# Performance work log

Hardware: AMD Instinct MI355X
Metric: run time of the kernel (lower is better)

Reference implementation:

```python
import jax, jax.numpy as jnp
import numpy as np

SIM_THRESHOLD = 0.7
EPS = 1e-8  # matches torch F.cosine_similarity eps

Q, M, D, C = 4096, 65536, 384, 128


def setup_inputs() -> dict:
    key = jax.random.key(0)
    k1, k2, k3 = jax.random.split(key, 3)
    query_embeddings = jax.random.normal(k1, (Q, D), dtype=jnp.float32)
    memory_embeddings = jax.random.normal(k2, (M, D), dtype=jnp.float32)
    # per-example one-hot-ish label vectors [M, C]
    memory_labels = jax.random.uniform(k3, (M, C), dtype=jnp.float32)
    return {
        "query_embeddings": query_embeddings,
        "memory_embeddings": memory_embeddings,
        "memory_labels": memory_labels,
    }


def _l2_normalize(x):
    n = jnp.sqrt(jnp.sum(x * x, axis=-1, keepdims=True))
    return x / jnp.maximum(n, EPS)


def reference(query_embeddings, memory_embeddings, memory_labels):
    # cosine similarity matrix [Q, M] via normalized GEMM
    qn = _l2_normalize(query_embeddings)          # [Q, D]
    mn = _l2_normalize(memory_embeddings)         # [M, D]
    sims = jnp.einsum("qd,md->qm", qn, mn)        # [Q, M]
    max_sim = jnp.max(sims, axis=1)               # [Q]
    max_idx = jnp.argmax(sims, axis=1)            # [Q]
    picked = memory_labels[max_idx]               # [Q, C] gather
    C_ = memory_labels.shape[1]
    uniform = jnp.full((1, C_), 1.0 / C_, dtype=picked.dtype)
    predictions = jnp.where((max_sim > SIM_THRESHOLD)[:, None], picked, uniform)
    return predictions
```

## Files before the change

kernel.cpp:

```cpp
#include <hip/hip_runtime.h>
#include <math.h>

#define QN 4096
#define MN 65536
#define DN 384
#define CN 128
#define NCHUNK 64
#define MROWS_PER_CHUNK (MN / NCHUNK)
#define MT_PER (MROWS_PER_CHUNK / 64)
#define BTILE_B (64 * DN)

typedef __attribute__((ext_vector_type(8))) int i32x8;
typedef __attribute__((ext_vector_type(4))) int i32x4;
typedef __attribute__((ext_vector_type(4))) float f32x4;

__device__ __forceinline__ unsigned char f2fp8(float f) {
  return (unsigned char)(__builtin_amdgcn_cvt_pk_fp8_f32(f, 0.f, 0, false) & 0xff);
}

__device__ __forceinline__ void async16(const void* g, void* l) {
  __builtin_amdgcn_global_load_lds(
      (const __attribute__((address_space(1))) unsigned int*)g,
      (__attribute__((address_space(3))) unsigned int*)l, 16, 0, 0);
}

__global__ __launch_bounds__(256) void nrm_kernel(const float* __restrict__ qe,
                                                  const float* __restrict__ me,
                                                  unsigned char* __restrict__ yq,
                                                  unsigned char* __restrict__ ym) {
  const int row = blockIdx.x * 4 + (threadIdx.x >> 6);
  const int lane = threadIdx.x & 63;
  const float* xr;
  unsigned char* yr;
  if (row < QN) {
    xr = qe + (size_t)row * DN;
    yr = yq + (size_t)row * DN;
  } else {
    xr = me + (size_t)(row - QN) * DN;
    yr = ym + (size_t)(row - QN) * DN;
  }
  float v[6];
  float ss = 0.f;
#pragma unroll
  for (int i = 0; i < 6; ++i) {
    v[i] = xr[lane + i * 64];
    ss += v[i] * v[i];
  }
#pragma unroll
  for (int m = 1; m < 64; m <<= 1) ss += __shfl_xor(ss, m);
  const float scale = 1.0f / fmaxf(sqrtf(ss), 1e-8f);
#pragma unroll
  for (int i = 0; i < 6; ++i) yr[lane + i * 64] = f2fp8(v[i] * scale);
}

__global__ __launch_bounds__(256, 2) void gemm_max_kernel(
    const unsigned char* __restrict__ qn8, const unsigned char* __restrict__ mn8,
    float* __restrict__ pmax) {
  __shared__ unsigned char Bs[2 * BTILE_B];
  __shared__ float smax[2][128];

  const int tid = threadIdx.x;
  const int wave = tid >> 6, lane = tid & 63;
  const int wr = wave >> 1, wc = wave & 1;
  const int quad = lane >> 4, l16 = lane & 15;
  const int r7 = l16 & 7;

  const int bid = blockIdx.y * gridDim.x + blockIdx.x;
  const int xcd = bid & 7;
  const int j = bid >> 3;
  const int ychunk = (xcd << 3) | (j >> 5);
  const int qrow0 = (j & 31) * 128;
  const int mchunk0 = ychunk * MROWS_PER_CHUNK;

  float rmax[16];
#pragma unroll
  for (int i = 0; i < 16; ++i) rmax[i] = -3.0e38f;

  {
    const unsigned char* abase = qn8 + (size_t)qrow0 * DN;
#pragma unroll
    for (int i = 0; i < 12; ++i) {
      const int ci = i * 256 + tid;
      const int row = ci / 24;
      const int jj = ci - row * 24;
      const int gj = (jj & 24) | ((jj ^ row) & 7);
      async16(abase + row * DN + gj * 16, &Bs[(i * 256 + wave * 64) * 16]);
    }
  }
  __syncthreads();
  i32x8 afr[3][4];
#pragma unroll
  for (int kc = 0; kc < 3; ++kc)
#pragma unroll
    for (int rt = 0; rt < 4; ++rt) {
      const unsigned char* p = &Bs[(wr * 64 + rt * 16 + l16) * DN];
      i32x4 lo = *(const i32x4*)&p[(kc * 8 + ((quad * 2 + 0) ^ r7)) * 16];
      i32x4 hi = *(const i32x4*)&p[(kc * 8 + ((quad * 2 + 1) ^ r7)) * 16];
      afr[kc][rt][0] = lo[0]; afr[kc][rt][1] = lo[1];
      afr[kc][rt][2] = lo[2]; afr[kc][rt][3] = lo[3];
      afr[kc][rt][4] = hi[0]; afr[kc][rt][5] = hi[1];
      afr[kc][rt][6] = hi[2]; afr[kc][rt][7] = hi[3];
    }
  __syncthreads();

  int srcoff[6];
#pragma unroll
  for (int i = 0; i < 6; ++i) {
    const int ci = i * 256 + tid;
    const int row = ci / 24;
    const int jj = ci - row * 24;
    const int gj = (jj & 24) | ((jj ^ row) & 7);
    srcoff[i] = row * DN + gj * 16;
  }

  const unsigned char* bchunk = mn8 + (size_t)mchunk0 * DN;
#pragma unroll
  for (int i = 0; i < 6; ++i)
    async16(bchunk + srcoff[i], &Bs[(i * 256 + wave * 64) * 16]);
#pragma unroll
  for (int i = 0; i < 6; ++i)
    async16(bchunk + BTILE_B + srcoff[i],
            &Bs[BTILE_B + (i * 256 + wave * 64) * 16]);

#pragma unroll 1
  for (int mt = 0; mt < MT_PER; ++mt) {
    if (mt == MT_PER - 1)
      asm volatile("s_waitcnt vmcnt(0)" ::: "memory");
    else
      asm volatile("s_waitcnt vmcnt(6)" ::: "memory");
    __builtin_amdgcn_s_barrier();
    __builtin_amdgcn_sched_barrier(0);

    const unsigned char* cur = &Bs[(mt & 1) * BTILE_B];

    i32x8 bfr[3][2];
#pragma unroll
    for (int kc = 0; kc < 3; ++kc)
#pragma unroll
      for (int ct = 0; ct < 2; ++ct) {
        const unsigned char* p = &cur[(wc * 32 + ct * 16 + l16) * DN];
        i32x4 lo = *(const i32x4*)&p[(kc * 8 + ((quad * 2 + 0) ^ r7)) * 16];
        i32x4 hi = *(const i32x4*)&p[(kc * 8 + ((quad * 2 + 1) ^ r7)) * 16];
        bfr[kc][ct][0] = lo[0]; bfr[kc][ct][1] = lo[1];
        bfr[kc][ct][2] = lo[2]; bfr[kc][ct][3] = lo[3];
        bfr[kc][ct][4] = hi[0]; bfr[kc][ct][5] = hi[1];
        bfr[kc][ct][6] = hi[2]; bfr[kc][ct][7] = hi[3];
      }

    asm volatile("s_waitcnt lgkmcnt(0)" ::: "memory");
    __builtin_amdgcn_sched_barrier(0);
    __builtin_amdgcn_s_barrier();

    if (mt + 2 < MT_PER) {
      unsigned char* nxt = (unsigned char*)cur;
      const unsigned char* nb = bchunk + (size_t)(mt + 2) * BTILE_B;
#pragma unroll
      for (int i = 0; i < 6; ++i)
        async16(nb + srcoff[i], &nxt[(i * 256 + wave * 64) * 16]);
    }

    f32x4 acc[4][2];
#pragma unroll
    for (int rt = 0; rt < 4; ++rt)
#pragma unroll
      for (int ct = 0; ct < 2; ++ct) acc[rt][ct] = (f32x4){0.f, 0.f, 0.f, 0.f};

    __builtin_amdgcn_s_setprio(1);
#pragma unroll
    for (int kc = 0; kc < 3; ++kc)
#pragma unroll
      for (int rt = 0; rt < 4; ++rt)
#pragma unroll
        for (int ct = 0; ct < 2; ++ct)
          acc[rt][ct] = __builtin_amdgcn_mfma_scale_f32_16x16x128_f8f6f4(
              afr[kc][rt], bfr[kc][ct], acc[rt][ct], 0, 0,
              0, 0x7f7f7f7f, 0, 0x7f7f7f7f);
    __builtin_amdgcn_s_setprio(0);

#pragma unroll
    for (int rt = 0; rt < 4; ++rt)
#pragma unroll
      for (int r = 0; r < 4; ++r) {
        const float v = fmaxf(acc[rt][0][r], acc[rt][1][r]);
        rmax[rt * 4 + r] = fmaxf(rmax[rt * 4 + r], v);
      }
  }

#pragma unroll
  for (int i = 0; i < 16; ++i) {
    float v = rmax[i];
    v = fmaxf(v, __shfl_xor(v, 1));
    v = fmaxf(v, __shfl_xor(v, 2));
    v = fmaxf(v, __shfl_xor(v, 4));
    v = fmaxf(v, __shfl_xor(v, 8));
    rmax[i] = v;
  }
  if (l16 == 0) {
#pragma unroll
    for (int rt = 0; rt < 4; ++rt)
#pragma unroll
      for (int r = 0; r < 4; ++r)
        smax[wc][wr * 64 + rt * 16 + quad * 4 + r] = rmax[rt * 4 + r];
  }
  __syncthreads();
  if (tid < 128) {
    const float v = fmaxf(smax[0][tid], smax[1][tid]);
    pmax[(size_t)(qrow0 + tid) * NCHUNK + ychunk] = v;
  }
}

__global__ __launch_bounds__(256) void decide_kernel(
    const float* __restrict__ pmax, const float* __restrict__ qe,
    const float* __restrict__ me, const float* __restrict__ labels,
    float* __restrict__ out) {
  const int q = blockIdx.x;
  const int t = threadIdx.x;
  __shared__ float smx;
  if (t < 64) {
    float v = pmax[(size_t)q * NCHUNK + t];
#pragma unroll
    for (int m = 1; m < 64; m <<= 1) v = fmaxf(v, __shfl_xor(v, m));
    if (t == 0) smx = v;
  }
  __syncthreads();
  if (smx <= 0.5f) {
    if (t < CN) out[(size_t)q * CN + t] = 1.0f / 128.0f;
    return;
  }
  __shared__ float sred[256];
  __shared__ int sidx[256];
  __shared__ float wsum[4];
  const float* qr = qe + (size_t)q * DN;
  float ss = 0.f;
  for (int i = t; i < DN; i += 256) ss += qr[i] * qr[i];
#pragma unroll
  for (int m = 1; m < 64; m <<= 1) ss += __shfl_xor(ss, m);
  if ((t & 63) == 0) wsum[t >> 6] = ss;
  __syncthreads();
  const float qnorm = fmaxf(sqrtf(wsum[0] + wsum[1] + wsum[2] + wsum[3]), 1e-8f);

  float best = -3.0e38f;
  int bidx = 0x7fffffff;
  for (int j = t; j < MN; j += 256) {
    const float* mr = me + (size_t)j * DN;
    float dot = 0.f, ms = 0.f;
    for (int k = 0; k < DN; ++k) {
      float a = qr[k], b = mr[k];
      dot += a * b;
      ms += b * b;
    }
    const float sim = dot / (qnorm * fmaxf(sqrtf(ms), 1e-8f));
    if (sim > best) { best = sim; bidx = j; }
  }
  sred[t] = best;
  sidx[t] = bidx;
  __syncthreads();
  for (int s = 128; s > 0; s >>= 1) {
    if (t < s) {
      const float ov = sred[t + s];
      const int oi = sidx[t + s];
      if (ov > sred[t] || (ov == sred[t] && oi < sidx[t])) {
        sred[t] = ov;
        sidx[t] = oi;
      }
    }
    __syncthreads();
  }
  const float mx = sred[0];
  const int mi = sidx[0];
  if (t < CN)
    out[(size_t)q * CN + t] =
        (mx > 0.7f) ? labels[(size_t)mi * CN + t] : (1.0f / 128.0f);
}

extern "C" void kernel_launch(void* const* d_in, const int* in_sizes, int n_in,
                              void* d_out, int out_size, void* d_ws,
                              size_t ws_size, hipStream_t stream) {
  const float* qe = (const float*)d_in[0];
  const float* me = (const float*)d_in[1];
  const float* lb = (const float*)d_in[2];
  float* out = (float*)d_out;

  char* ws = (char*)d_ws;
  const size_t OFF_QN = 0;
  const size_t OFF_MN = OFF_QN + (size_t)QN * DN;
  const size_t OFF_PMAX = OFF_MN + (size_t)MN * DN;
  unsigned char* qn8 = (unsigned char*)(ws + OFF_QN);
  unsigned char* mn8 = (unsigned char*)(ws + OFF_MN);
  float* pmax = (float*)(ws + OFF_PMAX);

  nrm_kernel<<<(QN + MN) / 4, 256, 0, stream>>>(qe, me, qn8, mn8);
  gemm_max_kernel<<<dim3(QN / 128, NCHUNK), 256, 0, stream>>>(qn8, mn8, pmax);
  decide_kernel<<<QN, 256, 0, stream>>>(pmax, qe, me, lb, out);
}
```

Measured before the change: 246.6 us.

## Triple-buffer B tiles in LDS and double-buffer B fragments in registers

```diff
diff --git a/kernel.cpp b/kernel.cpp
--- a/kernel.cpp
+++ b/kernel.cpp
@@ -9,6 +9,7 @@
 #define MROWS_PER_CHUNK (MN / NCHUNK)
 #define MT_PER (MROWS_PER_CHUNK / 64)
 #define BTILE_B (64 * DN)
+#define NBUF 3
 
 typedef __attribute__((ext_vector_type(8))) int i32x8;
 typedef __attribute__((ext_vector_type(4))) int i32x4;
@@ -56,7 +57,7 @@
 __global__ __launch_bounds__(256, 2) void gemm_max_kernel(
     const unsigned char* __restrict__ qn8, const unsigned char* __restrict__ mn8,
     float* __restrict__ pmax) {
-  __shared__ unsigned char Bs[2 * BTILE_B];
+  __shared__ unsigned char Bs[NBUF * BTILE_B];
   __shared__ float smax[2][128];
 
   const int tid = threadIdx.x;
@@ -115,76 +116,94 @@
 
   const unsigned char* bchunk = mn8 + (size_t)mchunk0 * DN;
 #pragma unroll
-  for (int i = 0; i < 6; ++i)
-    async16(bchunk + srcoff[i], &Bs[(i * 256 + wave * 64) * 16]);
-#pragma unroll
-  for (int i = 0; i < 6; ++i)
-    async16(bchunk + BTILE_B + srcoff[i],
-            &Bs[BTILE_B + (i * 256 + wave * 64) * 16]);
+  for (int t = 0; t < 3; ++t)
+#pragma unroll
+    for (int i = 0; i < 6; ++i)
+      async16(bchunk + (size_t)t * BTILE_B + srcoff[i],
+              &Bs[t * BTILE_B + (i * 256 + wave * 64) * 16]);
+
+  asm volatile("s_waitcnt vmcnt(12)" ::: "memory");
+  __builtin_amdgcn_s_barrier();
+  __builtin_amdgcn_sched_barrier(0);
+
+  i32x8 bfrA[3][2], bfrB[3][2];
+#pragma unroll
+  for (int kc = 0; kc < 3; ++kc)
+#pragma unroll
+    for (int ct = 0; ct < 2; ++ct) {
+      const unsigned char* p = &Bs[(wc * 32 + ct * 16 + l16) * DN];
+      i32x4 lo = *(const i32x4*)&p[(kc * 8 + ((quad * 2 + 0) ^ r7)) * 16];
+      i32x4 hi = *(const i32x4*)&p[(kc * 8 + ((quad * 2 + 1) ^ r7)) * 16];
+      bfrA[kc][ct][0] = lo[0]; bfrA[kc][ct][1] = lo[1];
+      bfrA[kc][ct][2] = lo[2]; bfrA[kc][ct][3] = lo[3];
+      bfrA[kc][ct][4] = hi[0]; bfrA[kc][ct][5] = hi[1];
+      bfrA[kc][ct][6] = hi[2]; bfrA[kc][ct][7] = hi[3];
+    }
+  asm volatile("s_waitcnt lgkmcnt(0)" ::: "memory");
+  __builtin_amdgcn_sched_barrier(0);
+  __builtin_amdgcn_s_barrier();
+
+#define GEMM_BODY(MT, CUR, NXT)                                               \
+  do {                                                                        \
+    const int mt_ = (MT);                                                     \
+    const int sb_ = mt_ % 3;                                                  \
+    const int rb_ = (mt_ + 1) % 3;                                            \
+    if (mt_ + 3 < MT_PER) {                                                   \
+      unsigned char* dst = &Bs[sb_ * BTILE_B];                                \
+      const unsigned char* nb = bchunk + (size_t)(mt_ + 3) * BTILE_B;         \
+      _Pragma("unroll") for (int i = 0; i < 6; ++i)                           \
+          async16(nb + srcoff[i], &dst[(i * 256 + wave * 64) * 16]);          \
+    }                                                                         \
+    if (mt_ + 3 < MT_PER)                                                     \
+      asm volatile("s_waitcnt vmcnt(12)" ::: "memory");                       \
+    else if (mt_ + 2 < MT_PER)                                                \
+      asm volatile("s_waitcnt vmcnt(6)" ::: "memory");                        \
+    else if (mt_ + 1 < MT_PER)                                                \
+      asm volatile("s_waitcnt vmcnt(0)" ::: "memory");                        \
+    __builtin_amdgcn_s_barrier();        \
+    __builtin_amdgcn_sched_barrier(0);                                        \
+    if (mt_ + 1 < MT_PER) {                                                   \
+      const unsigned char* cb = &Bs[rb_ * BTILE_B];                           \
+      _Pragma("unroll") for (int kc = 0; kc < 3; ++kc)                        \
+          _Pragma("unroll") for (int ct = 0; ct < 2; ++ct) {                  \
+        const unsigned char* p = &cb[(wc * 32 + ct * 16 + l16) * DN];         \
+        i32x4 lo = *(const i32x4*)&p[(kc * 8 + ((quad * 2 + 0) ^ r7)) * 16];  \
+        i32x4 hi = *(const i32x4*)&p[(kc * 8 + ((quad * 2 + 1) ^ r7)) * 16];  \
+        NXT[kc][ct][0] = lo[0]; NXT[kc][ct][1] = lo[1];                       \
+        NXT[kc][ct][2] = lo[2]; NXT[kc][ct][3] = lo[3];                       \
+        NXT[kc][ct][4] = hi[0]; NXT[kc][ct][5] = hi[1];                       \
+        NXT[kc][ct][6] = hi[2]; NXT[kc][ct][7] = hi[3];                       \
+      }                                                                       \
+    }                                                                         \
+    f32x4 acc[4][2];                                                          \
+    _Pragma("unroll") for (int rt = 0; rt < 4; ++rt)                          \
+        _Pragma("unroll") for (int ct = 0; ct < 2; ++ct)                      \
+            acc[rt][ct] = (f32x4){0.f, 0.f, 0.f, 0.f};                        \
+    __builtin_amdgcn_s_setprio(1);                                            \
+    _Pragma("unroll") for (int kc = 0; kc < 3; ++kc)                          \
+        _Pragma("unroll") for (int rt = 0; rt < 4; ++rt)                      \
+            _Pragma("unroll") for (int ct = 0; ct < 2; ++ct)                  \
+                acc[rt][ct] =                                                 \
+                    __builtin_amdgcn_mfma_scale_f32_16x16x128_f8f6f4(         \
+                        afr[kc][rt], CUR[kc][ct], acc[rt][ct], 0, 0,          \
+                        0, 0x7f7f7f7f, 0, 0x7f7f7f7f);                        \
+    __builtin_amdgcn_s_setprio(0);                                            \
+    _Pragma("unroll") for (int rt = 0; rt < 4; ++rt)                          \
+        _Pragma("unroll") for (int r = 0; r < 4; ++r) {                       \
+      const float v = fmaxf(acc[rt][0][r], acc[rt][1][r]);                    \
+      rmax[rt * 4 + r] = fmaxf(rmax[rt * 4 + r], v);                          \
+    }                                                                         \
+    asm volatile("s_waitcnt lgkmcnt(0)" ::: "memory");                        \
+    __builtin_amdgcn_sched_barrier(0);                                        \
+    __builtin_amdgcn_s_barrier();    \
+  } while (0)
 
 #pragma unroll 1
-  for (int mt = 0; mt < MT_PER; ++mt) {
-    if (mt == MT_PER - 1)
-      asm volatile("s_waitcnt vmcnt(0)" ::: "memory");
-    else
-      asm volatile("s_waitcnt vmcnt(6)" ::: "memory");
-    __builtin_amdgcn_s_barrier();
-    __builtin_amdgcn_sched_barrier(0);
-
-    const unsigned char* cur = &Bs[(mt & 1) * BTILE_B];
-
-    i32x8 bfr[3][2];
-#pragma unroll
-    for (int kc = 0; kc < 3; ++kc)
-#pragma unroll
-      for (int ct = 0; ct < 2; ++ct) {
-        const unsigned char* p = &cur[(wc * 32 + ct * 16 + l16) * DN];
-        i32x4 lo = *(const i32x4*)&p[(kc * 8 + ((quad * 2 + 0) ^ r7)) * 16];
-        i32x4 hi = *(const i32x4*)&p[(kc * 8 + ((quad * 2 + 1) ^ r7)) * 16];
-        bfr[kc][ct][0] = lo[0]; bfr[kc][ct][1] = lo[1];
-        bfr[kc][ct][2] = lo[2]; bfr[kc][ct][3] = lo[3];
-        bfr[kc][ct][4] = hi[0]; bfr[kc][ct][5] = hi[1];
-        bfr[kc][ct][6] = hi[2]; bfr[kc][ct][7] = hi[3];
-      }
-
-    asm volatile("s_waitcnt lgkmcnt(0)" ::: "memory");
-    __builtin_amdgcn_sched_barrier(0);
-    __builtin_amdgcn_s_barrier();
-
-    if (mt + 2 < MT_PER) {
-      unsigned char* nxt = (unsigned char*)cur;
-      const unsigned char* nb = bchunk + (size_t)(mt + 2) * BTILE_B;
-#pragma unroll
-      for (int i = 0; i < 6; ++i)
-        async16(nb + srcoff[i], &nxt[(i * 256 + wave * 64) * 16]);
-    }
-
-    f32x4 acc[4][2];
-#pragma unroll
-    for (int rt = 0; rt < 4; ++rt)
-#pragma unroll
-      for (int ct = 0; ct < 2; ++ct) acc[rt][ct] = (f32x4){0.f, 0.f, 0.f, 0.f};
-
-    __builtin_amdgcn_s_setprio(1);
-#pragma unroll
-    for (int kc = 0; kc < 3; ++kc)
-#pragma unroll
-      for (int rt = 0; rt < 4; ++rt)
-#pragma unroll
-        for (int ct = 0; ct < 2; ++ct)
-          acc[rt][ct] = __builtin_amdgcn_mfma_scale_f32_16x16x128_f8f6f4(
-              afr[kc][rt], bfr[kc][ct], acc[rt][ct], 0, 0,
-              0, 0x7f7f7f7f, 0, 0x7f7f7f7f);
-    __builtin_amdgcn_s_setprio(0);
-
-#pragma unroll
-    for (int rt = 0; rt < 4; ++rt)
-#pragma unroll
-      for (int r = 0; r < 4; ++r) {
-        const float v = fmaxf(acc[rt][0][r], acc[rt][1][r]);
-        rmax[rt * 4 + r] = fmaxf(rmax[rt * 4 + r], v);
-      }
-  }
+  for (int mtp = 0; mtp < MT_PER; mtp += 2) {
+    GEMM_BODY(mtp, bfrA, bfrB);
+    GEMM_BODY(mtp + 1, bfrB, bfrA);
+  }
+#undef GEMM_BODY
 
 #pragma unroll
   for (int i = 0; i < 16; ++i) {
```

Measured after the change: 454.9 us. 1.84x slower.
